# Performance work log

Hardware: AMD Instinct MI355X
Metric: run time of the kernel (lower is better)

## Reference

```python
import jax, jax.numpy as jnp
import numpy as np

# Nominal per-type footprint heights used only to pick a STATIC scatter window
# (must upper-bound the node_size values produced in setup_inputs()).
_MAX_SX = {1: 1.0, 2: 1.0, 3: 1.0}
_MAX_SY = {1: 1.0, 2: 2.5, 3: 5.0}


def _raster(stm, t, sx, sy, width, height, nbx, nby):
    """Rasterize all sites of type t (each a sx-by-sy rect at integer (rw,cl))
    into an (nbx,nby) capacity histogram with fractional bin overlap."""
    binW = width / nbx
    binH = height / nby
    KX = int(np.ceil(_MAX_SX[t] / binW)) + 1  # static window of candidate bins in x
    KY = int(np.ceil(_MAX_SY[t] / binH)) + 1  # static window of candidate bins in y
    idx = jnp.arange(width * height, dtype=jnp.int32)
    r = (idx // height).astype(jnp.float32)  # site x coordinate (rw)
    c = (idx % height).astype(jnp.float32)   # site y coordinate (cl)
    mask = stm == t
    iLo = jnp.floor(r / binW).astype(jnp.int32)
    jLo = jnp.floor(c / binH).astype(jnp.int32)
    cap = jnp.zeros((nbx, nby), jnp.float32)
    for di in range(KX):
        i = iLo + di
        w = jnp.minimum((i + 1) * binW, r + sx) - jnp.maximum(i * binW, r)
        okx = (i <= nbx - 1) & (w > 0)
        ic = jnp.minimum(i, nbx - 1)
        for dj in range(KY):
            j = jLo + dj
            h = jnp.minimum((j + 1) * binH, c + sy) - jnp.maximum(j * binH, c)
            contrib = jnp.where(mask & okx & (j <= nby - 1) & (h > 0), w * h, 0.0)
            cap = cap.at[ic, jnp.minimum(j, nby - 1)].add(contrib)
    return cap


def setup_inputs() -> dict:
    key = jax.random.key(0)
    W = H = 2048
    NBX = NBY = 2048
    stm = jax.random.randint(key, (W * H,), 0, 4, dtype=jnp.int32)
    node_size_x = jnp.ones((4,), jnp.float32)                       # all site types 1 wide
    node_size_y = jnp.array([1.0, 1.0, 2.5, 5.0], jnp.float32)      # SLICE/SLICE/DSP/RAM heights
    return {
        "site_type_map": stm,
        "node_size_x": node_size_x,
        "node_size_y": node_size_y,
        "width": W, "height": H,
        "num_bins_x": NBX, "num_bins_y": NBY,
        "xl": 0, "xh": W, "yl": 0, "yh": H,
    }


def reference(site_type_map, node_size_x, node_size_y, width, height,
              num_bins_x, num_bins_y, xl, xh, yl, yh):
    cap0 = _raster(site_type_map, 1, node_size_x[0], node_size_y[0],
                   width, height, num_bins_x, num_bins_y)
    cap2 = _raster(site_type_map, 2, node_size_x[2], node_size_y[2],
                   width, height, num_bins_x, num_bins_y)
    cap3 = _raster(site_type_map, 3, node_size_x[3], node_size_y[3],
                   width, height, num_bins_x, num_bins_y)
    binArea = ((xh - xl) / num_bins_x) * ((yh - yl) / num_bins_y)
    # binCapMap1 aliases binCapMap0 in the torch code
    return (binArea - cap0, binArea - cap0, binArea - cap2, binArea - cap3)
```

## Files before the change

kernel.cpp:

```cpp
#include <hip/hip_runtime.h>


typedef float v4f __attribute__((ext_vector_type(4)));

__global__ __launch_bounds__(256) void demand_map_kernel(
    const int* __restrict__ stm,
    const float* __restrict__ nsx,
    const float* __restrict__ nsy,
    const int* __restrict__ heightP,
    const int* __restrict__ nbxP, const int* __restrict__ nbyP,
    const int* __restrict__ xlP, const int* __restrict__ xhP,
    const int* __restrict__ ylP, const int* __restrict__ yhP,
    float* __restrict__ out,
    int total)
{
    const int n4   = total >> 2;
    const int wid  = threadIdx.x >> 6;
    const int lane = threadIdx.x & 63;
    const int base = blockIdx.x * 128;
    const int g0 = base + lane;
    const int g1 = g0 + 64;
    if (g0 >= n4) return;
    const bool do1 = (g1 < n4);

    const int height = *heightP;
    const float binArea =
        ((float)(*xhP - *xlP) / (float)(*nbxP)) *
        ((float)(*yhP - *ylP) / (float)(*nbyP));

    const int t    = (wid <= 1) ? 1 : wid;
    const int sidx = (wid <= 1) ? 0 : wid;
    const float wx = fminf(nsx[sidx], 1.0f);
    const float sy = nsy[sidx];
    float w[5];
    #pragma unroll
    for (int k = 0; k < 5; ++k) w[k] = fminf(fmaxf(sy - (float)k, 0.0f), 1.0f);

    const int4* stm4 = (const int4*)stm;

    const int4 curA = stm4[g0];
    int4 prevA = make_int4(0, 0, 0, 0);
    if (((g0 << 2) % height) != 0) prevA = stm4[g0 - 1];
    int4 curB = make_int4(0, 0, 0, 0), prevB = make_int4(0, 0, 0, 0);
    if (do1) {
        curB = stm4[g1];
        if (((g1 << 2) % height) != 0) prevB = stm4[g1 - 1];
    }

    v4f* out4 = (v4f*)out;
    const int mapOff = wid * n4;

    #pragma unroll
    for (int it = 0; it < 2; ++it) {
        if (it == 1 && !do1) break;
        const int g = (it == 0) ? g0 : g1;
        const int4 cur  = (it == 0) ? curA  : curB;
        const int4 prev = (it == 0) ? prevA : prevB;

        int s[8] = { prev.x, prev.y, prev.z, prev.w,
                     cur.x,  cur.y,  cur.z,  cur.w };

        float o[4];
        #pragma unroll
        for (int e = 0; e < 4; ++e) {
            float c = 0.0f;
            #pragma unroll
            for (int k = 0; k < 5; ++k)
                c += w[k] * (float)(s[4 + e - k] == t);
            o[e] = binArea - wx * c;
        }

        const v4f v = { o[0], o[1], o[2], o[3] };
        __builtin_nontemporal_store(v, &out4[mapOff + g]);
    }
}

extern "C" void kernel_launch(void* const* d_in, const int* in_sizes, int n_in,
                              void* d_out, int out_size, void* d_ws, size_t ws_size,
                              hipStream_t stream) {
    const int*   stm = (const int*)  d_in[0];
    const float* nsx = (const float*)d_in[1];
    const float* nsy = (const float*)d_in[2];
    const int* heightP = (const int*)d_in[4];
    const int* nbxP    = (const int*)d_in[5];
    const int* nbyP    = (const int*)d_in[6];
    const int* xlP     = (const int*)d_in[7];
    const int* xhP     = (const int*)d_in[8];
    const int* ylP     = (const int*)d_in[9];
    const int* yhP     = (const int*)d_in[10];

    float* out = (float*)d_out;
    const int total = in_sizes[0];
    const int n4 = total >> 2;
    const int blocks = (n4 + 127) / 128;

    demand_map_kernel<<<blocks, 256, 0, stream>>>(
        stm, nsx, nsy, heightP, nbxP, nbyP, xlP, xhP, ylP, yhP, out, total);
}
```

Baseline: 18.40 us.

## Use persistent grid of 1024 blocks with per-map slices and prefetch loop

Replaces the one-block-per-128-groups launch, where the four warps of a block handled the four output maps, with a fixed grid of 1024 blocks. Each block owns one output map and one contiguous slice of site groups, and its threads stride through that slice with a software-prefetched next load. This cuts block launch overhead and overlaps the next input load with the current store. In exchange, each input element is now read by four separate blocks instead of once per block, and load balance depends on the slice size.

New measurement: 19.67 us. +6.9%, slower.

```diff
diff --git a/kernel.cpp b/kernel.cpp
--- a/kernel.cpp
+++ b/kernel.cpp
@@ -14,22 +14,21 @@
     float* __restrict__ out,
     int total)
 {
-    const int n4   = total >> 2;
-    const int wid  = threadIdx.x >> 6;
-    const int lane = threadIdx.x & 63;
-    const int base = blockIdx.x * 128;
-    const int g0 = base + lane;
-    const int g1 = g0 + 64;
-    if (g0 >= n4) return;
-    const bool do1 = (g1 < n4);
+    const int n4  = total >> 2;
+    const int map = blockIdx.x >> 8;
+    const int slc = blockIdx.x & 255;
+    const int sliceGroups = (n4 + 255) >> 8;
+    const int base = slc * sliceGroups;
+    const int end  = min(base + sliceGroups, n4);
+    if (base >= n4) return;
 
     const int height = *heightP;
     const float binArea =
         ((float)(*xhP - *xlP) / (float)(*nbxP)) *
         ((float)(*yhP - *ylP) / (float)(*nbyP));
 
-    const int t    = (wid <= 1) ? 1 : wid;
-    const int sidx = (wid <= 1) ? 0 : wid;
+    const int t    = (map <= 1) ? 1 : map;
+    const int sidx = (map <= 1) ? 0 : map;
     const float wx = fminf(nsx[sidx], 1.0f);
     const float sy = nsy[sidx];
     float w[5];
@@ -37,25 +36,25 @@
     for (int k = 0; k < 5; ++k) w[k] = fminf(fmaxf(sy - (float)k, 0.0f), 1.0f);
 
     const int4* stm4 = (const int4*)stm;
+    v4f* out4 = (v4f*)out;
+    const long long mapOff = (long long)map * n4;
 
-    const int4 curA = stm4[g0];
-    int4 prevA = make_int4(0, 0, 0, 0);
-    if (((g0 << 2) % height) != 0) prevA = stm4[g0 - 1];
-    int4 curB = make_int4(0, 0, 0, 0), prevB = make_int4(0, 0, 0, 0);
-    if (do1) {
-        curB = stm4[g1];
-        if (((g1 << 2) % height) != 0) prevB = stm4[g1 - 1];
+    int g = base + (int)threadIdx.x;
+    int4 cur  = make_int4(0, 0, 0, 0);
+    int4 prev = make_int4(0, 0, 0, 0);
+    if (g < end) {
+        cur = stm4[g];
+        if (((g << 2) % height) != 0) prev = stm4[g - 1];
     }
 
-    v4f* out4 = (v4f*)out;
-    const int mapOff = wid * n4;
-
-    #pragma unroll
-    for (int it = 0; it < 2; ++it) {
-        if (it == 1 && !do1) break;
-        const int g = (it == 0) ? g0 : g1;
-        const int4 cur  = (it == 0) ? curA  : curB;
-        const int4 prev = (it == 0) ? prevA : prevB;
+    while (g < end) {
+        const int gn = g + 256;
+        int4 ncur  = make_int4(0, 0, 0, 0);
+        int4 nprev = make_int4(0, 0, 0, 0);
+        if (gn < end) {
+            ncur = stm4[gn];
+            if (((gn << 2) % height) != 0) nprev = stm4[gn - 1];
+        }
 
         int s[8] = { prev.x, prev.y, prev.z, prev.w,
                      cur.x,  cur.y,  cur.z,  cur.w };
@@ -72,6 +71,8 @@
 
         const v4f v = { o[0], o[1], o[2], o[3] };
         __builtin_nontemporal_store(v, &out4[mapOff + g]);
+
+        cur = ncur; prev = nprev; g = gn;
     }
 }
 
@@ -91,9 +92,7 @@
 
     float* out = (float*)d_out;
     const int total = in_sizes[0];
-    const int n4 = total >> 2;
-    const int blocks = (n4 + 127) / 128;
 
-    demand_map_kernel<<<blocks, 256, 0, stream>>>(
+    demand_map_kernel<<<1024, 256, 0, stream>>>(
         stm, nsx, nsy, heightP, nbxP, nbyP, xlP, xhP, ylP, yhP, out, total);
 }
```
